# Optimization experiments

Hardware: AMD Instinct MI355X
Metric: run time of the kernel (lower is better)

The kernel has to match this reference:

```python
import jax, jax.numpy as jnp
import numpy as np

V, E, H, B, T = 32000, 256, 512, 16, 256


def setup_inputs() -> dict:
    key = jax.random.key(0)
    ks = jax.random.split(key, 12)
    s = 1.0 / np.sqrt(H)  # torch nn.RNN init range
    u = lambda k, shape: jax.random.uniform(k, shape, jnp.float32, -s, s)
    return dict(
        X=jax.random.randint(ks[0], (B, T), 0, V),
        emb=jax.random.normal(ks[1], (V, E), jnp.float32),
        W_ih0=u(ks[2], (H, E)), W_hh0=u(ks[3], (H, H)),
        b_ih0=u(ks[4], (H,)), b_hh0=u(ks[5], (H,)),
        W_ih1=u(ks[6], (H, H)), W_hh1=u(ks[7], (H, H)),
        b_ih1=u(ks[8], (H,)), b_hh1=u(ks[9], (H,)),
        W_fc=u(ks[10], (V, H)), b_fc=u(ks[11], (V,)),
    )


def _rnn_layer(x, W_ih, W_hh, b_ih, b_hh):
    """Elman RNN layer, batch_first. x: [B,T,D] -> (outputs [B,T,H], h_T [B,H]).
    h_t = tanh(x_t @ W_ih^T + b_ih + h_{t-1} @ W_hh^T + b_hh), h_0 = 0."""
    # Precompute the input projection for all timesteps (one big GEMM).
    xp = jnp.einsum('btd,hd->bth', x, W_ih) + b_ih + b_hh  # [B,T,H]

    def step(h, xt):
        h = jnp.tanh(xt + h @ W_hh.T)
        return h, h

    h0 = jnp.zeros((x.shape[0], W_hh.shape[0]), x.dtype)
    hT, ys = jax.lax.scan(step, h0, jnp.swapaxes(xp, 0, 1))  # scan over T
    return jnp.swapaxes(ys, 0, 1), hT


def reference(X, emb, W_ih0, W_hh0, b_ih0, b_hh0,
              W_ih1, W_hh1, b_ih1, b_hh1, W_fc, b_fc):
    x = emb[X]  # [B,T,E]
    out1, h1 = _rnn_layer(x, W_ih0, W_hh0, b_ih0, b_hh0)
    out2, h2 = _rnn_layer(out1, W_ih1, W_hh1, b_ih1, b_hh1)
    logits = jnp.einsum('bth,vh->btv', out2, W_fc) + b_fc  # [B,T,V]
    hidden = jnp.stack([h1, h2], axis=0)  # [n_layers, B, H]
    return logits, hidden, out2
```

## Files before the change

### kernel.cpp

```cpp
#include <hip/hip_runtime.h>
#include <hip/hip_fp16.h>

#define BB 16
#define TT 256
#define HH 512
#define EE 256
#define VV 32000

using half8  = __attribute__((ext_vector_type(8))) _Float16;
using float4v = __attribute__((ext_vector_type(4))) float;
typedef unsigned long long u64;

#define WS_WFC16   0u
#define WS_XG      32768000u
#define WS_WIH0    34865152u
#define WS_XP0     35127296u
#define WS_H0EX    43515904u
#define WS_H1EX    47710208u
#define WS_OUT2F16 51904512u
#define WS_FLAGS   56098816u
#define WS_NEEDED  56115200u

__global__ void init_flags_k(unsigned* f) {
    f[blockIdx.x * 256 + threadIdx.x] = 0u;
}

__global__ void cvt_f32_f16_k(const float* __restrict__ s, _Float16* __restrict__ d, int n) {
    int i = blockIdx.x * 256 + threadIdx.x;
    if (i < n) d[i] = (_Float16)s[i];
}

__global__ void gather_embed_k(const int* __restrict__ X, const float* __restrict__ emb,
                               _Float16* __restrict__ xg) {
    int m = blockIdx.x;
    int e = threadIdx.x;
    int row = X[m];
    xg[m * EE + e] = (_Float16)emb[(size_t)row * EE + e];
}

template <bool PERM>
__global__ __launch_bounds__(256)
void gemm_f16_k(const _Float16* __restrict__ A, const _Float16* __restrict__ Bm,
                const float* __restrict__ bias0, const float* __restrict__ bias1,
                float* __restrict__ C, int M, int N, int K) {
    __shared__ _Float16 As[128][40];
    __shared__ _Float16 Bs[128][40];
    const int tid = threadIdx.x;
    const int l = tid & 63, w = tid >> 6;
    const int ntiles = N >> 7;
    const int m0 = (blockIdx.x / ntiles) << 7;
    const int n0 = (blockIdx.x % ntiles) << 7;
    const int wr = (w >> 1) << 6, wc = (w & 1) << 6;
    const int lrow = tid >> 1, lseg = (tid & 1) << 4;
    const int ar = l & 15, ak = (l >> 4) << 3;

    float4v acc[4][4] = {};

    for (int kt = 0; kt < K; kt += 32) {
        const _Float16* ga = A  + (size_t)(m0 + lrow) * K + kt + lseg;
        const _Float16* gb = Bm + (size_t)(n0 + lrow) * K + kt + lseg;
        *(int4*)&As[lrow][lseg]     = *(const int4*)ga;
        *(int4*)&As[lrow][lseg + 8] = *(const int4*)(ga + 8);
        *(int4*)&Bs[lrow][lseg]     = *(const int4*)gb;
        *(int4*)&Bs[lrow][lseg + 8] = *(const int4*)(gb + 8);
        __syncthreads();

        half8 af[4], bf[4];
#pragma unroll
        for (int m = 0; m < 4; ++m) af[m] = *(half8*)&As[wr + m * 16 + ar][ak];
#pragma unroll
        for (int n = 0; n < 4; ++n) bf[n] = *(half8*)&Bs[wc + n * 16 + ar][ak];
#pragma unroll
        for (int m = 0; m < 4; ++m)
#pragma unroll
            for (int n = 0; n < 4; ++n)
                acc[m][n] = __builtin_amdgcn_mfma_f32_16x16x32_f16(af[m], bf[n], acc[m][n], 0, 0, 0);
        __syncthreads();
    }

#pragma unroll
    for (int m = 0; m < 4; ++m) {
#pragma unroll
        for (int n = 0; n < 4; ++n) {
            const int col = n0 + wc + n * 16 + (l & 15);
            float bv = (bias0 ? bias0[col] : 0.f) + (bias1 ? bias1[col] : 0.f);
#pragma unroll
            for (int r = 0; r < 4; ++r) {
                const int row = m0 + wr + m * 16 + ((l >> 4) << 2) + r;
                float v = acc[m][n][r] + bv;
                if (PERM) {
                    int t = row & 255, b = row >> 8;
                    C[(size_t)((t << 4) + b) * HH + col] = v;
                } else {
                    C[(size_t)row * N + col] = v;
                }
            }
        }
    }
}

__global__ __launch_bounds__(256)
void rnn_fused_k(const float* __restrict__ Whh0, const float* __restrict__ Wih1,
                 const float* __restrict__ Whh1,
                 const float* __restrict__ bih1, const float* __restrict__ bhh1,
                 const float* __restrict__ xp0,
                 unsigned* __restrict__ h0ex,
                 unsigned* __restrict__ h1ex,
                 _Float16* __restrict__ out2f16,
                 float* __restrict__ out_hidden,
                 float* __restrict__ out2f32,
                 unsigned* __restrict__ flags) {
    const int tid = threadIdx.x, l = tid & 63, w = tid >> 6;
    const int layer = blockIdx.x >> 3, blk = blockIdx.x & 7;
    const int mycol = blk * 64 + w * 16 + (l & 15);
    const int kq = (l >> 4) << 3;

    __shared__ _Float16 hA[16][520];
    __shared__ _Float16 hB[16][520];

    half8 wA[16], wB[16];
    {
        const float* WhhL = layer ? Whh1 : Whh0;
#pragma unroll
        for (int kk = 0; kk < 16; ++kk) {
            const float* src = WhhL + (size_t)mycol * HH + kk * 32 + kq;
            half8 h;
#pragma unroll
            for (int i = 0; i < 8; ++i) h[i] = (_Float16)src[i];
            wA[kk] = h;
        }
        if (layer) {
#pragma unroll
            for (int kk = 0; kk < 16; ++kk) {
                const float* src = Wih1 + (size_t)mycol * HH + kk * 32 + kq;
                half8 h;
#pragma unroll
                for (int i = 0; i < 8; ++i) h[i] = (_Float16)src[i];
                wB[kk] = h;
            }
        }
    }
    const float bsum = layer ? (bih1[mycol] + bhh1[mycol]) : 0.f;

    unsigned* flags0 = flags;
    unsigned* flags1 = flags + TT * 8;

    for (int t = 0; t < TT; ++t) {
        if (w == 0) {
            for (;;) {
                unsigned v = 1;
                if (layer == 0) {
                    if (t > 0 && l < 8)
                        v = __hip_atomic_load(&flags0[(t - 1) * 8 + l], __ATOMIC_ACQUIRE, __HIP_MEMORY_SCOPE_AGENT);
                } else {
                    if (l < 8)
                        v = __hip_atomic_load(&flags0[t * 8 + l], __ATOMIC_ACQUIRE, __HIP_MEMORY_SCOPE_AGENT);
                    else if (l < 16 && t > 0)
                        v = __hip_atomic_load(&flags1[(t - 1) * 8 + (l - 8)], __ATOMIC_ACQUIRE, __HIP_MEMORY_SCOPE_AGENT);
                }
                if (__all(v != 0)) break;
                __builtin_amdgcn_s_sleep(8);
            }
        }
        __syncthreads();

        const u64* pA = nullptr;
        const u64* pB = nullptr;
        if (layer == 0) { if (t > 0) pA = (const u64*)h0ex + (size_t)(t - 1) * 2048; }
        else { pA = (const u64*)h0ex + (size_t)t * 2048; if (t > 0) pB = (const u64*)h1ex + (size_t)(t - 1) * 2048; }
        if (pA) {
#pragma unroll
            for (int j = 0; j < 8; ++j) {
                int c = j * 256 + tid;
                u64 d = __hip_atomic_load(&pA[c], __ATOMIC_RELAXED, __HIP_MEMORY_SCOPE_AGENT);
                *(u64*)&hA[c >> 7][(c & 127) << 2] = d;
            }
        }
        if (pB) {
#pragma unroll
            for (int j = 0; j < 8; ++j) {
                int c = j * 256 + tid;
                u64 d = __hip_atomic_load(&pB[c], __ATOMIC_RELAXED, __HIP_MEMORY_SCOPE_AGENT);
                *(u64*)&hB[c >> 7][(c & 127) << 2] = d;
            }
        }
        __syncthreads();

        float4v acc = {0.f, 0.f, 0.f, 0.f};
        if (layer) {
#pragma unroll
            for (int kk = 0; kk < 16; ++kk) {
                half8 a = *(half8*)&hA[l & 15][kk * 32 + kq];
                acc = __builtin_amdgcn_mfma_f32_16x16x32_f16(a, wB[kk], acc, 0, 0, 0);
            }
            if (t > 0) {
#pragma unroll
                for (int kk = 0; kk < 16; ++kk) {
                    half8 a = *(half8*)&hB[l & 15][kk * 32 + kq];
                    acc = __builtin_amdgcn_mfma_f32_16x16x32_f16(a, wA[kk], acc, 0, 0, 0);
                }
            }
        } else if (t > 0) {
#pragma unroll
            for (int kk = 0; kk < 16; ++kk) {
                half8 a = *(half8*)&hA[l & 15][kk * 32 + kq];
                acc = __builtin_amdgcn_mfma_f32_16x16x32_f16(a, wA[kk], acc, 0, 0, 0);
            }
        }

        float hv[4];
#pragma unroll
        for (int r = 0; r < 4; ++r) {
            int b = ((l >> 4) << 2) + r;
            float x = layer ? bsum : xp0[(size_t)((t << 4) + b) * HH + mycol];
            hv[r] = tanhf(x + acc[r]);
        }

        unsigned* dst = (layer ? h1ex : h0ex) + (size_t)t * 4096;
#pragma unroll
        for (int r = 0; r < 4; ++r) {
            int b = ((l >> 4) << 2) + r;
            unsigned short mu = __builtin_bit_cast(unsigned short, (_Float16)hv[r]);
            int ov = __shfl_xor((int)mu, 1, 64);
            if ((l & 1) == 0) {
                unsigned val = (unsigned)mu | ((unsigned)ov << 16);
                __hip_atomic_store(&dst[b * 256 + (mycol >> 1)], val, __ATOMIC_RELAXED, __HIP_MEMORY_SCOPE_AGENT);
            }
            if (layer) {
                size_t row = (size_t)(b << 8) + t;
                out2f32[row * HH + mycol] = hv[r];
                out2f16[row * HH + mycol] = (_Float16)hv[r];
            }
            if (t == TT - 1) out_hidden[(size_t)(layer * BB + b) * HH + mycol] = hv[r];
        }

        asm volatile("s_waitcnt vmcnt(0)" ::: "memory");
        __syncthreads();
        if (tid == 0)
            __hip_atomic_store(&(layer ? flags1 : flags0)[t * 8 + blk], 1u,
                               __ATOMIC_RELEASE, __HIP_MEMORY_SCOPE_AGENT);
    }
}

extern "C" void kernel_launch(void* const* d_in, const int* in_sizes, int n_in,
                              void* d_out, int out_size, void* d_ws, size_t ws_size,
                              hipStream_t stream) {
    if (ws_size < WS_NEEDED) return;

    const int*   X     = (const int*)d_in[0];
    const float* emb   = (const float*)d_in[1];
    const float* Wih0  = (const float*)d_in[2];
    const float* Whh0  = (const float*)d_in[3];
    const float* bih0  = (const float*)d_in[4];
    const float* bhh0  = (const float*)d_in[5];
    const float* Wih1  = (const float*)d_in[6];
    const float* Whh1  = (const float*)d_in[7];
    const float* bih1  = (const float*)d_in[8];
    const float* bhh1  = (const float*)d_in[9];
    const float* Wfc   = (const float*)d_in[10];
    const float* bfc   = (const float*)d_in[11];

    char* ws = (char*)d_ws;
    _Float16* Wfc16   = (_Float16*)(ws + WS_WFC16);
    _Float16* xg      = (_Float16*)(ws + WS_XG);
    _Float16* Wih0f16 = (_Float16*)(ws + WS_WIH0);
    float*    xp0     = (float*)(ws + WS_XP0);
    unsigned* h0ex    = (unsigned*)(ws + WS_H0EX);
    unsigned* h1ex    = (unsigned*)(ws + WS_H1EX);
    _Float16* o2f16   = (_Float16*)(ws + WS_OUT2F16);
    unsigned* flags   = (unsigned*)(ws + WS_FLAGS);

    float* logits     = (float*)d_out;
    float* hidden     = (float*)d_out + (size_t)BB * TT * VV;
    float* out2       = hidden + 2 * BB * HH;

    hipLaunchKernelGGL(init_flags_k, dim3(16), dim3(256), 0, stream, flags);
    hipLaunchKernelGGL(gather_embed_k, dim3(BB * TT), dim3(256), 0, stream, X, emb, xg);
    hipLaunchKernelGGL(cvt_f32_f16_k, dim3((HH * EE) / 256), dim3(256), 0, stream, Wih0, Wih0f16, HH * EE);
    hipLaunchKernelGGL(cvt_f32_f16_k, dim3((VV * HH) / 256), dim3(256), 0, stream, Wfc, Wfc16, VV * HH);

    hipLaunchKernelGGL((gemm_f16_k<true>), dim3((4096 / 128) * (HH / 128)), dim3(256), 0, stream,
                       xg, Wih0f16, bih0, bhh0, xp0, 4096, HH, EE);

    hipLaunchKernelGGL(rnn_fused_k, dim3(16), dim3(256), 0, stream,
                       Whh0, Wih1, Whh1, bih1, bhh1, xp0, h0ex, h1ex, o2f16, hidden, out2, flags);

    hipLaunchKernelGGL((gemm_f16_k<false>), dim3((4096 / 128) * (VV / 128)), dim3(256), 0, stream,
                       o2f16, Wfc16, bfc, nullptr, logits, 4096, VV, HH);
}
```

Baseline: 1.868 ms.

## Run each RNN layer in one workgroup and pipeline layer-1 input projection

The 16-block RNN kernel, which used cross-block flag handshakes every timestep, becomes a 34-block kernel. Each layer's recurrence runs in a single 512-thread workgroup that keeps W_hh in registers and LDS, and the hidden state is exchanged through LDS with block barriers. Another 32 blocks compute the layer-1 input projection per timestep from layer-0 outputs and hand it over through per-step flags. This takes global-memory flag polling off the serial recurrence, adds a fast exp/rcp tanh, and prefetches the next step's input. The trade-off is fewer blocks doing the serial work, more inter-block signalling for xp1, and tanh_fast precision that differs from tanhf.

```diff
diff --git a/kernel.cpp b/kernel.cpp
--- a/kernel.cpp
+++ b/kernel.cpp
@@ -7,19 +7,20 @@
 #define EE 256
 #define VV 32000
 
-using half8  = __attribute__((ext_vector_type(8))) _Float16;
+using half8   = __attribute__((ext_vector_type(8))) _Float16;
 using float4v = __attribute__((ext_vector_type(4))) float;
 typedef unsigned long long u64;
 
 #define WS_WFC16   0u
 #define WS_XG      32768000u
 #define WS_WIH0    34865152u
-#define WS_XP0     35127296u
-#define WS_H0EX    43515904u
-#define WS_H1EX    47710208u
-#define WS_OUT2F16 51904512u
-#define WS_FLAGS   56098816u
-#define WS_NEEDED  56115200u
+#define WS_WIH1    35127296u
+#define WS_XP0     35651584u
+#define WS_XP1     44040192u
+#define WS_H0EX    52428800u
+#define WS_OUT2F16 56623104u
+#define WS_FLAGS   60817408u
+#define WS_NEEDED  60833792u
 
 __global__ void init_flags_k(unsigned* f) {
     f[blockIdx.x * 256 + threadIdx.x] = 0u;
@@ -99,146 +100,252 @@
     }
 }
 
-__global__ __launch_bounds__(256)
-void rnn_fused_k(const float* __restrict__ Whh0, const float* __restrict__ Wih1,
-                 const float* __restrict__ Whh1,
-                 const float* __restrict__ bih1, const float* __restrict__ bhh1,
-                 const float* __restrict__ xp0,
-                 unsigned* __restrict__ h0ex,
-                 unsigned* __restrict__ h1ex,
-                 _Float16* __restrict__ out2f16,
-                 float* __restrict__ out_hidden,
-                 float* __restrict__ out2f32,
-                 unsigned* __restrict__ flags) {
-    const int tid = threadIdx.x, l = tid & 63, w = tid >> 6;
-    const int layer = blockIdx.x >> 3, blk = blockIdx.x & 7;
-    const int mycol = blk * 64 + w * 16 + (l & 15);
-    const int kq = (l >> 4) << 3;
-
-    __shared__ _Float16 hA[16][520];
-    __shared__ _Float16 hB[16][520];
-
-    half8 wA[16], wB[16];
-    {
-        const float* WhhL = layer ? Whh1 : Whh0;
-#pragma unroll
-        for (int kk = 0; kk < 16; ++kk) {
-            const float* src = WhhL + (size_t)mycol * HH + kk * 32 + kq;
-            half8 h;
-#pragma unroll
-            for (int i = 0; i < 8; ++i) h[i] = (_Float16)src[i];
-            wA[kk] = h;
-        }
-        if (layer) {
-#pragma unroll
-            for (int kk = 0; kk < 16; ++kk) {
-                const float* src = Wih1 + (size_t)mycol * HH + kk * 32 + kq;
+__device__ __forceinline__ float tanh_fast(float x) {
+    float e = __expf(2.0f * x);
+    return 1.0f - 2.0f * __builtin_amdgcn_rcpf(e + 1.0f);
+}
+
+__global__ __launch_bounds__(512, 2)
+void rnn_pipe_k(const float* __restrict__ Whh0, const float* __restrict__ Whh1,
+                const _Float16* __restrict__ Wih1f16,
+                const float* __restrict__ bih1, const float* __restrict__ bhh1,
+                const float* __restrict__ xp0, float* __restrict__ xp1,
+                unsigned* __restrict__ h0ex,
+                _Float16* __restrict__ out2f16, float* __restrict__ out_hidden,
+                float* __restrict__ out2f32,
+                unsigned* __restrict__ flags0, unsigned* __restrict__ flag1x)
+{
+    __shared__ _Float16 hbuf[16][520];
+    __shared__ _Float16 wlds[8 * 4 * 4 * 64 * 8];
+
+    const int tid = threadIdx.x;
+    const int l = tid & 63, w = tid >> 6;
+    const int lq = l >> 4;
+    const int kq = lq << 3;
+    const int c15 = l & 15;
+    const int bi = blockIdx.x;
+
+    if (bi < 2) {
+        const int layer = bi;
+        const float* Whh = layer ? Whh1 : Whh0;
+
+        half8 wf[4][12];
+#pragma unroll
+        for (int ct = 0; ct < 4; ++ct) {
+            const int col = w * 64 + ct * 16 + c15;
+            const float* wrow = Whh + (size_t)col * HH;
+#pragma unroll
+            for (int kt = 0; kt < 16; ++kt) {
+                const float* s = wrow + kt * 32 + kq;
+                float4v f0 = *(const float4v*)s;
+                float4v f1 = *(const float4v*)(s + 4);
                 half8 h;
 #pragma unroll
-                for (int i = 0; i < 8; ++i) h[i] = (_Float16)src[i];
-                wB[kk] = h;
-            }
-        }
-    }
-    const float bsum = layer ? (bih1[mycol] + bhh1[mycol]) : 0.f;
-
-    unsigned* flags0 = flags;
-    unsigned* flags1 = flags + TT * 8;
-
-    for (int t = 0; t < TT; ++t) {
-        if (w == 0) {
+                for (int i = 0; i < 4; ++i) { h[i] = (_Float16)f0[i]; h[i + 4] = (_Float16)f1[i]; }
+                if (kt < 12) wf[ct][kt] = h;
+                else *(half8*)&wlds[((((w * 4 + ct) * 4) + (kt - 12)) * 64 + l) * 8] = h;
+            }
+        }
+
+        float4v acc[4], accn[4];
+        if (layer == 0) {
+#pragma unroll
+            for (int ct = 0; ct < 4; ++ct) {
+                const int col = w * 64 + ct * 16 + c15;
+#pragma unroll
+                for (int r = 0; r < 4; ++r)
+                    acc[ct][r] = xp0[(size_t)(lq * 4 + r) * HH + col];
+            }
+        } else {
+            while (!__hip_atomic_load(&flag1x[0], __ATOMIC_ACQUIRE, __HIP_MEMORY_SCOPE_AGENT))
+                __builtin_amdgcn_s_sleep(2);
+#pragma unroll
+            for (int ct = 0; ct < 4; ++ct) {
+                const int col = w * 64 + ct * 16 + c15;
+#pragma unroll
+                for (int r = 0; r < 4; ++r)
+                    acc[ct][r] = __hip_atomic_load(&xp1[(size_t)(lq * 4 + r) * HH + col],
+                                                   __ATOMIC_RELAXED, __HIP_MEMORY_SCOPE_AGENT);
+            }
+        }
+        __syncthreads();
+
+        for (int t = 0; t < TT; ++t) {
+            if (t > 0) {
+#pragma unroll
+                for (int kt = 0; kt < 16; ++kt) {
+                    half8 a = *(const half8*)&hbuf[c15][kt * 32 + kq];
+                    half8 b0, b1, b2, b3;
+                    if (kt < 12) {
+                        b0 = wf[0][kt]; b1 = wf[1][kt]; b2 = wf[2][kt]; b3 = wf[3][kt];
+                    } else {
+                        b0 = *(const half8*)&wlds[((((w * 4 + 0) * 4) + (kt - 12)) * 64 + l) * 8];
+                        b1 = *(const half8*)&wlds[((((w * 4 + 1) * 4) + (kt - 12)) * 64 + l) * 8];
+                        b2 = *(const half8*)&wlds[((((w * 4 + 2) * 4) + (kt - 12)) * 64 + l) * 8];
+                        b3 = *(const half8*)&wlds[((((w * 4 + 3) * 4) + (kt - 12)) * 64 + l) * 8];
+                    }
+                    acc[0] = __builtin_amdgcn_mfma_f32_16x16x32_f16(a, b0, acc[0], 0, 0, 0);
+                    acc[1] = __builtin_amdgcn_mfma_f32_16x16x32_f16(a, b1, acc[1], 0, 0, 0);
+                    acc[2] = __builtin_amdgcn_mfma_f32_16x16x32_f16(a, b2, acc[2], 0, 0, 0);
+                    acc[3] = __builtin_amdgcn_mfma_f32_16x16x32_f16(a, b3, acc[3], 0, 0, 0);
+                }
+            }
+
+            if (layer == 0 && t > 0) {
+                asm volatile("s_waitcnt vmcnt(0)" ::: "memory");
+                if (l == 0)
+                    __hip_atomic_store(&flags0[(t - 1) * 8 + w], 1u,
+                                       __ATOMIC_RELAXED, __HIP_MEMORY_SCOPE_AGENT);
+            }
+
+            if (t + 1 < TT) {
+                if (layer == 0) {
+#pragma unroll
+                    for (int ct = 0; ct < 4; ++ct) {
+                        const int col = w * 64 + ct * 16 + c15;
+#pragma unroll
+                        for (int r = 0; r < 4; ++r)
+                            accn[ct][r] = xp0[(size_t)((t + 1) * 16 + lq * 4 + r) * HH + col];
+                    }
+                } else {
+                    while (!__hip_atomic_load(&flag1x[t + 1], __ATOMIC_ACQUIRE, __HIP_MEMORY_SCOPE_AGENT))
+                        __builtin_amdgcn_s_sleep(2);
+#pragma unroll
+                    for (int ct = 0; ct < 4; ++ct) {
+                        const int col = w * 64 + ct * 16 + c15;
+#pragma unroll
+                        for (int r = 0; r < 4; ++r)
+                            accn[ct][r] = __hip_atomic_load(&xp1[(size_t)((t + 1) * 16 + lq * 4 + r) * HH + col],
+                                                            __ATOMIC_RELAXED, __HIP_MEMORY_SCOPE_AGENT);
+                    }
+                }
+            }
+
+            unsigned pk[4][4];
+#pragma unroll
+            for (int ct = 0; ct < 4; ++ct) {
+                const int col = w * 64 + ct * 16 + c15;
+#pragma unroll
+                for (int r = 0; r < 4; ++r) {
+                    const int b = lq * 4 + r;
+                    float hv = tanh_fast(acc[ct][r]);
+                    if (layer)
+                        out2f32[((size_t)(b << 8) + t) * HH + col] = hv;
+                    if (t == TT - 1)
+                        out_hidden[(size_t)(layer * BB + b) * HH + col] = hv;
+                    unsigned short mu = __builtin_bit_cast(unsigned short, (_Float16)hv);
+                    int ov = __shfl_xor((int)mu, 1, 64);
+                    pk[ct][r] = (unsigned)mu | ((unsigned)ov << 16);
+                }
+            }
+
+            if (layer == 0) {
+                unsigned* dst = h0ex + (size_t)t * 4096;
+#pragma unroll
+                for (int ct = 0; ct < 4; ++ct) {
+                    const int col = w * 64 + ct * 16 + c15;
+#pragma unroll
+                    for (int r = 0; r < 4; ++r)
+                        if ((l & 1) == 0)
+                            __hip_atomic_store(&dst[(lq * 4 + r) * 256 + (col >> 1)], pk[ct][r],
+                                               __ATOMIC_RELAXED, __HIP_MEMORY_SCOPE_AGENT);
+                }
+            } else {
+#pragma unroll
+                for (int ct = 0; ct < 4; ++ct) {
+                    const int col = w * 64 + ct * 16 + c15;
+#pragma unroll
+                    for (int r = 0; r < 4; ++r)
+                        if ((l & 1) == 0)
+                            *(unsigned*)&out2f16[((size_t)((lq * 4 + r) << 8) + t) * HH + col] = pk[ct][r];
+                }
+            }
+
+            asm volatile("" ::: "memory");
+            __builtin_amdgcn_s_barrier();
+            asm volatile("" ::: "memory");
+
+#pragma unroll
+            for (int ct = 0; ct < 4; ++ct) {
+                const int col = w * 64 + ct * 16 + c15;
+#pragma unroll
+                for (int r = 0; r < 4; ++r)
+                    if ((l & 1) == 0)
+                        *(unsigned*)&hbuf[lq * 4 + r][col] = pk[ct][r];
+            }
+            asm volatile("s_waitcnt lgkmcnt(0)" ::: "memory");
+            __builtin_amdgcn_s_barrier();
+            asm volatile("" ::: "memory");
+
+            if (t + 1 < TT) {
+#pragma unroll
+                for (int ct = 0; ct < 4; ++ct) acc[ct] = accn[ct];
+            }
+        }
+
+        if (layer == 0) {
+            asm volatile("s_waitcnt vmcnt(0)" ::: "memory");
+            if (l == 0)
+                __hip_atomic_store(&flags0[(TT - 1) * 8 + w], 1u,
+                                   __ATOMIC_RELAXED, __HIP_MEMORY_SCOPE_AGENT);
+        }
+    } else {
+        const int stripe = bi - 2;
+        float bsum[4];
+#pragma unroll
+        for (int ct = 0; ct < 4; ++ct) {
+            const int col = w * 64 + ct * 16 + c15;
+            bsum[ct] = bih1[col] + bhh1[col];
+        }
+        const int base64 = c15 * 128 + lq * 2;
+
+        for (int j = 0; j < 8; ++j) {
+            const int t = stripe + 32 * j;
             for (;;) {
-                unsigned v = 1;
-                if (layer == 0) {
-                    if (t > 0 && l < 8)
-                        v = __hip_atomic_load(&flags0[(t - 1) * 8 + l], __ATOMIC_ACQUIRE, __HIP_MEMORY_SCOPE_AGENT);
-                } else {
-                    if (l < 8)
-                        v = __hip_atomic_load(&flags0[t * 8 + l], __ATOMIC_ACQUIRE, __HIP_MEMORY_SCOPE_AGENT);
-                    else if (l < 16 && t > 0)
-                        v = __hip_atomic_load(&flags1[(t - 1) * 8 + (l - 8)], __ATOMIC_ACQUIRE, __HIP_MEMORY_SCOPE_AGENT);
-                }
+                unsigned v = 1u;
+                if (l < 8)
+                    v = __hip_atomic_load(&flags0[t * 8 + l], __ATOMIC_ACQUIRE, __HIP_MEMORY_SCOPE_AGENT);
                 if (__all(v != 0)) break;
-                __builtin_amdgcn_s_sleep(8);
-            }
-        }
-        __syncthreads();
-
-        const u64* pA = nullptr;
-        const u64* pB = nullptr;
-        if (layer == 0) { if (t > 0) pA = (const u64*)h0ex + (size_t)(t - 1) * 2048; }
-        else { pA = (const u64*)h0ex + (size_t)t * 2048; if (t > 0) pB = (const u64*)h1ex + (size_t)(t - 1) * 2048; }
-        if (pA) {
-#pragma unroll
-            for (int j = 0; j < 8; ++j) {
-                int c = j * 256 + tid;
-                u64 d = __hip_atomic_load(&pA[c], __ATOMIC_RELAXED, __HIP_MEMORY_SCOPE_AGENT);
-                *(u64*)&hA[c >> 7][(c & 127) << 2] = d;
-            }
-        }
-        if (pB) {
-#pragma unroll
-            for (int j = 0; j < 8; ++j) {
-                int c = j * 256 + tid;
-                u64 d = __hip_atomic_load(&pB[c], __ATOMIC_RELAXED, __HIP_MEMORY_SCOPE_AGENT);
-                *(u64*)&hB[c >> 7][(c & 127) << 2] = d;
-            }
-        }
-        __syncthreads();
-
-        float4v acc = {0.f, 0.f, 0.f, 0.f};
-        if (layer) {
-#pragma unroll
-            for (int kk = 0; kk < 16; ++kk) {
-                half8 a = *(half8*)&hA[l & 15][kk * 32 + kq];
-                acc = __builtin_amdgcn_mfma_f32_16x16x32_f16(a, wB[kk], acc, 0, 0, 0);
-            }
-            if (t > 0) {
-#pragma unroll
-                for (int kk = 0; kk < 16; ++kk) {
-                    half8 a = *(half8*)&hB[l & 15][kk * 32 + kq];
-                    acc = __builtin_amdgcn_mfma_f32_16x16x32_f16(a, wA[kk], acc, 0, 0, 0);
-                }
-            }
-        } else if (t > 0) {
-#pragma unroll
-            for (int kk = 0; kk < 16; ++kk) {
-                half8 a = *(half8*)&hA[l & 15][kk * 32 + kq];
-                acc = __builtin_amdgcn_mfma_f32_16x16x32_f16(a, wA[kk], acc, 0, 0, 0);
-            }
-        }
-
-        float hv[4];
-#pragma unroll
-        for (int r = 0; r < 4; ++r) {
-            int b = ((l >> 4) << 2) + r;
-            float x = layer ? bsum : xp0[(size_t)((t << 4) + b) * HH + mycol];
-            hv[r] = tanhf(x + acc[r]);
-        }
-
-        unsigned* dst = (layer ? h1ex : h0ex) + (size_t)t * 4096;
-#pragma unroll
-        for (int r = 0; r < 4; ++r) {
-            int b = ((l >> 4) << 2) + r;
-            unsigned short mu = __builtin_bit_cast(unsigned short, (_Float16)hv[r]);
-            int ov = __shfl_xor((int)mu, 1, 64);
-            if ((l & 1) == 0) {
-                unsigned val = (unsigned)mu | ((unsigned)ov << 16);
-                __hip_atomic_store(&dst[b * 256 + (mycol >> 1)], val, __ATOMIC_RELAXED, __HIP_MEMORY_SCOPE_AGENT);
-            }
-            if (layer) {
-                size_t row = (size_t)(b << 8) + t;
-                out2f32[row * HH + mycol] = hv[r];
-                out2f16[row * HH + mycol] = (_Float16)hv[r];
-            }
-            if (t == TT - 1) out_hidden[(size_t)(layer * BB + b) * HH + mycol] = hv[r];
-        }
-
-        asm volatile("s_waitcnt vmcnt(0)" ::: "memory");
-        __syncthreads();
-        if (tid == 0)
-            __hip_atomic_store(&(layer ? flags1 : flags0)[t * 8 + blk], 1u,
-                               __ATOMIC_RELEASE, __HIP_MEMORY_SCOPE_AGENT);
+                __builtin_amdgcn_s_sleep(2);
+            }
+            half8 af[16];
+            const u64* pA = (const u64*)h0ex + (size_t)t * 2048;
+#pragma unroll
+            for (int kt = 0; kt < 16; ++kt) {
+                u64 d0 = __hip_atomic_load(pA + base64 + kt * 8,     __ATOMIC_RELAXED, __HIP_MEMORY_SCOPE_AGENT);
+                u64 d1 = __hip_atomic_load(pA + base64 + kt * 8 + 1, __ATOMIC_RELAXED, __HIP_MEMORY_SCOPE_AGENT);
+                union { u64 u[2]; half8 h; } cv;
+                cv.u[0] = d0; cv.u[1] = d1;
+                af[kt] = cv.h;
+            }
+            float4v acc[4];
+#pragma unroll
+            for (int ct = 0; ct < 4; ++ct) {
+                acc[ct][0] = bsum[ct]; acc[ct][1] = bsum[ct];
+                acc[ct][2] = bsum[ct]; acc[ct][3] = bsum[ct];
+            }
+#pragma unroll
+            for (int ct = 0; ct < 4; ++ct) {
+                const int col = w * 64 + ct * 16 + c15;
+                const _Float16* wp = Wih1f16 + (size_t)col * HH + kq;
+#pragma unroll
+                for (int kt = 0; kt < 16; ++kt) {
+                    half8 bf = *(const half8*)(wp + kt * 32);
+                    acc[ct] = __builtin_amdgcn_mfma_f32_16x16x32_f16(af[kt], bf, acc[ct], 0, 0, 0);
+                }
+            }
+#pragma unroll
+            for (int ct = 0; ct < 4; ++ct) {
+                const int col = w * 64 + ct * 16 + c15;
+#pragma unroll
+                for (int r = 0; r < 4; ++r)
+                    __hip_atomic_store(&xp1[(size_t)(t * 16 + lq * 4 + r) * HH + col], acc[ct][r],
+                                       __ATOMIC_RELAXED, __HIP_MEMORY_SCOPE_AGENT);
+            }
+            __syncthreads();
+            if (tid == 0)
+                __hip_atomic_store(&flag1x[t], 1u, __ATOMIC_RELEASE, __HIP_MEMORY_SCOPE_AGENT);
+        }
     }
 }
 
@@ -264,26 +371,30 @@
     _Float16* Wfc16   = (_Float16*)(ws + WS_WFC16);
     _Float16* xg      = (_Float16*)(ws + WS_XG);
     _Float16* Wih0f16 = (_Float16*)(ws + WS_WIH0);
+    _Float16* Wih1f16 = (_Float16*)(ws + WS_WIH1);
     float*    xp0     = (float*)(ws + WS_XP0);
+    float*    xp1     = (float*)(ws + WS_XP1);
     unsigned* h0ex    = (unsigned*)(ws + WS_H0EX);
-    unsigned* h1ex    = (unsigned*)(ws + WS_H1EX);
     _Float16* o2f16   = (_Float16*)(ws + WS_OUT2F16);
-    unsigned* flags   = (unsigned*)(ws + WS_FLAGS);
+    unsigned* flags0  = (unsigned*)(ws + WS_FLAGS);
+    unsigned* flag1x  = flags0 + TT * 8;
 
     float* logits     = (float*)d_out;
     float* hidden     = (float*)d_out + (size_t)BB * TT * VV;
     float* out2       = hidden + 2 * BB * HH;
 
-    hipLaunchKernelGGL(init_flags_k, dim3(16), dim3(256), 0, stream, flags);
+    hipLaunchKernelGGL(init_flags_k, dim3(9), dim3(256), 0, stream, flags0);
     hipLaunchKernelGGL(gather_embed_k, dim3(BB * TT), dim3(256), 0, stream, X, emb, xg);
     hipLaunchKernelGGL(cvt_f32_f16_k, dim3((HH * EE) / 256), dim3(256), 0, stream, Wih0, Wih0f16, HH * EE);
+    hipLaunchKernelGGL(cvt_f32_f16_k, dim3((HH * HH) / 256), dim3(256), 0, stream, Wih1, Wih1f16, HH * HH);
     hipLaunchKernelGGL(cvt_f32_f16_k, dim3((VV * HH) / 256), dim3(256), 0, stream, Wfc, Wfc16, VV * HH);
 
     hipLaunchKernelGGL((gemm_f16_k<true>), dim3((4096 / 128) * (HH / 128)), dim3(256), 0, stream,
                        xg, Wih0f16, bih0, bhh0, xp0, 4096, HH, EE);
 
-    hipLaunchKernelGGL(rnn_fused_k, dim3(16), dim3(256), 0, stream,
-                       Whh0, Wih1, Whh1, bih1, bhh1, xp0, h0ex, h1ex, o2f16, hidden, out2, flags);
+    hipLaunchKernelGGL(rnn_pipe_k, dim3(34), dim3(512), 0, stream,
+                       Whh0, Whh1, Wih1f16, bih1, bhh1, xp0, xp1,
+                       h0ex, o2f16, hidden, out2, flags0, flag1x);
 
     hipLaunchKernelGGL((gemm_f16_k<false>), dim3((4096 / 128) * (VV / 128)), dim3(256), 0, stream,
                        o2f16, Wfc16, bfc, nullptr, logits, 4096, VV, HH);
```

New measurement: 1.989 ms. 6.5% more time.
